# Kernel tuning notes

Hardware: AMD Instinct MI355X
Metric: run time of the kernel (lower is better)

The kernel has to match this reference:

```python
import jax, jax.numpy as jnp
import numpy as np

B, N, M, J, D, PF = 4, 131072, 10475, 55, 64, 486


def setup_inputs() -> dict:
    key = jax.random.key(0)
    ks = jax.random.split(key, 16)
    return {
        "pts": jax.random.normal(ks[0], (B, N, 3), jnp.float32),
        "betas": jax.random.normal(ks[1], (B, 10), jnp.float32),
        "pose_feature": jax.random.normal(ks[2], (B, PF), jnp.float32),
        "init_spdir": jax.random.normal(ks[3], (M, 3, 10), jnp.float32),
        "init_podir": jax.random.normal(ks[4], (PF, 3 * M), jnp.float32),
        "init_faces": jax.random.randint(ks[5], (N, 3), 0, M, jnp.int32),
        "tfs_A": jax.random.normal(ks[6], (B, J, 4, 4), jnp.float32),
        "tfs_inv": jax.random.normal(ks[7], (1, J, 4, 4), jnp.float32),
        "poseoff_cano": jax.random.normal(ks[8], (1, N, 3), jnp.float32),
        "lbsw": jax.random.uniform(ks[9], (1, N, J), jnp.float32),
        "lbs_voxel": jax.random.uniform(ks[10], (1, J, D, D, D), jnp.float32),
        "vox_scale": jnp.ones((1, 1, 3), jnp.float32),
        "vox_offset": jnp.zeros((1, 1, 3), jnp.float32),
        "mask": jax.random.randint(ks[11], (B, N), 0, 2, jnp.int32),
    }


def _trilinear(vox, x, scale, offset):
    # vox: [J,D,D,D], x: [b,n,3] -> [b,n,J] trilinearly interpolated weights
    nj, nd = vox.shape[0], vox.shape[-1]
    g = jnp.clip(x * scale + offset, -1.0, 1.0)          # normalized coords
    t = (g + 1.0) * 0.5 * (nd - 1)                        # voxel coords
    i0 = jnp.clip(jnp.floor(t), 0, nd - 2).astype(jnp.int32)
    f = t - i0                                            # fractional part
    vf = vox.reshape(nj, -1)                              # [J, D^3]
    out = jnp.zeros(x.shape[:-1] + (nj,), x.dtype)
    for dx in (0, 1):
        for dy in (0, 1):
            for dz in (0, 1):
                ix = i0[..., 0] + dx
                iy = i0[..., 1] + dy
                iz = i0[..., 2] + dz
                wgt = ((f[..., 0] if dx else 1.0 - f[..., 0]) *
                       (f[..., 1] if dy else 1.0 - f[..., 1]) *
                       (f[..., 2] if dz else 1.0 - f[..., 2]))
                fid = (ix * nd + iy) * nd + iz            # flat voxel index [b,n]
                out = out + wgt[..., None] * jnp.moveaxis(vf[:, fid], 0, -1)
    return out


def reference(pts, betas, pose_feature, init_spdir, init_podir, init_faces,
              tfs_A, tfs_inv, poseoff_cano, lbsw, lbs_voxel, vox_scale,
              vox_offset, mask):
    b, n, _ = pts.shape
    # blend-shape offsets on template vertices
    shape_full = jnp.einsum('bl,mkl->bmk', betas, init_spdir)      # [b,M,3]
    pose_full = (pose_feature @ init_podir).reshape(b, -1, 3)      # [b,M,3]
    # face-vertex gather then average over the 3 vertices of each face
    shape_off = shape_full[:, init_faces].mean(axis=2)             # [b,F,3]
    pose_off = pose_full[:, init_faces].mean(axis=2)               # [b,F,3]
    x = pts + shape_off + pose_off - poseoff_cano                  # canonical pts + offsets
    # voxel-grid skinning-weight lookup at canonical points
    w_vox = _trilinear(lbs_voxel[0], pts, vox_scale, vox_offset)   # [b,n,J]
    w = jnp.where(mask[..., None] > 0, lbsw, w_vox)
    w = w / jnp.clip(w.sum(-1, keepdims=True), 1e-8)
    # per-point blended transforms: A @ A_inv_template
    tfs = tfs_A @ tfs_inv                                          # [b,J,4,4]
    T = jnp.einsum('bnj,bjrc->bnrc', w, tfs)                       # [b,n,4,4]
    xh = jnp.concatenate([x, jnp.ones_like(x[..., :1])], axis=-1)
    posed = jnp.einsum('bnrc,bnc->bnr', T, xh)[..., :3]
    return posed.reshape(b, n, 1, 3), T
```

## Files before the change

kernel.cpp:

```cpp
#include <hip/hip_runtime.h>

#define B_  4
#define N_  131072
#define J_  55
#define JP_ 56
#define D_  64
#define D3_ 262144
#define PF_ 486
#define COLS_ 31425

#define GZ_ 2048
#define OZ_ 123
#define PZ_ 14336

#define BL16(u) __uint_as_float((u) << 16)
#define BH16(u) __uint_as_float((u) & 0xffff0000u)

typedef float f4a __attribute__((ext_vector_type(4), aligned(4)));

__device__ __forceinline__ unsigned short f2bf(float v) {
    unsigned u = __float_as_uint(v);
    u += 0x7fffu + ((u >> 16) & 1u);
    return (unsigned short)(u >> 16);
}

__device__ __forceinline__ void stage_tfs_bf16(int b, int tid,
                                               const float* __restrict__ A,
                                               const float* __restrict__ Ainv,
                                               unsigned* __restrict__ dst) {
#pragma unroll
    for (int base = 0; base < 448; base += 256) {
        int idx = base + tid;
        if (idx < 448) {
            int j = idx >> 3, pp = idx & 7;
            float e0 = 0.f, e1 = 0.f;
            if (j < J_) {
                int r = pp >> 1, c0 = (pp & 1) * 2;
#pragma unroll
                for (int k = 0; k < 4; ++k) {
                    float av = A[((b * J_ + j) * 4 + r) * 4 + k];
                    e0 += av * Ainv[(j * 4 + k) * 4 + c0];
                    e1 += av * Ainv[(j * 4 + k) * 4 + c0 + 1];
                }
            }
            dst[idx] = (unsigned)f2bf(e0) | ((unsigned)f2bf(e1) << 16);
        }
    }
}

#define UNP16(t, q0, q1)                                        \
    t[0]  = BL16(q0.x); t[1]  = BH16(q0.x);                     \
    t[2]  = BL16(q0.y); t[3]  = BH16(q0.y);                     \
    t[4]  = BL16(q0.z); t[5]  = BH16(q0.z);                     \
    t[6]  = BL16(q0.w); t[7]  = BH16(q0.w);                     \
    t[8]  = BL16(q1.x); t[9]  = BH16(q1.x);                     \
    t[10] = BL16(q1.y); t[11] = BH16(q1.y);                     \
    t[12] = BL16(q1.z); t[13] = BH16(q1.z);                     \
    t[14] = BL16(q1.w); t[15] = BH16(q1.w);

__global__ __launch_bounds__(256) void k_prelude(
    const float* __restrict__ A, const float* __restrict__ Ainv,
    const float* __restrict__ vox,
    uint4* __restrict__ Gtb, float* __restrict__ Stb,
    const float* __restrict__ pf, const float* __restrict__ podir,
    const float* __restrict__ betas, const float* __restrict__ spdir,
    float* __restrict__ off_full,
    const float* __restrict__ lbsw, unsigned* __restrict__ lbswP32) {
    int bx = blockIdx.x;
    int tid = threadIdx.x;

    if (bx < GZ_) {
        __shared__ unsigned stfsb[448];
        int b = (bx & 7) >> 1;
        int chunk = ((bx >> 3) << 1) | (bx & 1);
        stage_tfs_bf16(b, tid, A, Ainv, stfsb);
        __syncthreads();

        int v0 = chunk * 512 + tid;
        float g0[16], g1[16];
#pragma unroll
        for (int r = 0; r < 16; ++r) { g0[r] = 0.f; g1[r] = 0.f; }
        float s0 = 0.f, s1 = 0.f;
        const uint4* s16 = (const uint4*)stfsb;
        float wa[5][2], wb[5][2];
#pragma unroll
        for (int k = 0; k < 5; ++k) {
            wa[k][0] = vox[(size_t)k * D3_ + v0];
            wa[k][1] = vox[(size_t)k * D3_ + v0 + 256];
        }
        for (int j0 = 0; j0 < J_; j0 += 5) {
            if (j0 + 5 < J_) {
#pragma unroll
                for (int k = 0; k < 5; ++k) {
                    wb[k][0] = vox[(size_t)(j0 + 5 + k) * D3_ + v0];
                    wb[k][1] = vox[(size_t)(j0 + 5 + k) * D3_ + v0 + 256];
                }
            }
#pragma unroll
            for (int k = 0; k < 5; ++k) {
                int j = j0 + k;
                uint4 q0 = s16[j * 2], q1 = s16[j * 2 + 1];
                float t[16];
                UNP16(t, q0, q1)
                float w0 = wa[k][0], w1 = wa[k][1];
                s0 += w0; s1 += w1;
#pragma unroll
                for (int r = 0; r < 16; ++r) {
                    g0[r] += w0 * t[r];
                    g1[r] += w1 * t[r];
                }
            }
#pragma unroll
            for (int k = 0; k < 5; ++k) {
                wa[k][0] = wb[k][0]; wa[k][1] = wb[k][1];
            }
        }
        if (b == 0) { Stb[v0] = s0; Stb[v0 + 256] = s1; }
#pragma unroll
        for (int m = 0; m < 2; ++m) {
            float* g = m ? g1 : g0;
            int v = v0 + m * 256;
            unsigned gw[8];
#pragma unroll
            for (int k = 0; k < 8; ++k)
                gw[k] = (unsigned)f2bf(g[2 * k]) |
                        ((unsigned)f2bf(g[2 * k + 1]) << 16);
            uint4* gp = Gtb + ((size_t)b * D3_ + v) * 2;
            gp[0] = make_uint4(gw[0], gw[1], gw[2], gw[3]);
            gp[1] = make_uint4(gw[4], gw[5], gw[6], gw[7]);
        }
    } else if (bx < GZ_ + OZ_) {
        int col = (bx - GZ_) * 256 + tid;
        if (col >= COLS_) return;
        float a0 = 0.f, a1 = 0.f, a2 = 0.f, a3 = 0.f;
        {
            float sp[10];
#pragma unroll
            for (int l = 0; l < 10; ++l) sp[l] = spdir[col * 10 + l];
#pragma unroll
            for (int l = 0; l < 10; ++l) {
                a0 += betas[0 * 10 + l] * sp[l];
                a1 += betas[1 * 10 + l] * sp[l];
                a2 += betas[2 * 10 + l] * sp[l];
                a3 += betas[3 * 10 + l] * sp[l];
            }
        }
        int p = 0;
        for (; p + 16 <= PF_; p += 16) {
            float v16[16];
#pragma unroll
            for (int k = 0; k < 16; ++k)
                v16[k] = podir[(size_t)(p + k) * COLS_ + col];
#pragma unroll
            for (int k = 0; k < 16; ++k) {
                a0 += pf[0 * PF_ + p + k] * v16[k];
                a1 += pf[1 * PF_ + p + k] * v16[k];
                a2 += pf[2 * PF_ + p + k] * v16[k];
                a3 += pf[3 * PF_ + p + k] * v16[k];
            }
        }
        for (; p < PF_; ++p) {
            float v = podir[(size_t)p * COLS_ + col];
            a0 += pf[0 * PF_ + p] * v;
            a1 += pf[1 * PF_ + p] * v;
            a2 += pf[2 * PF_ + p] * v;
            a3 += pf[3 * PF_ + p] * v;
        }
        off_full[0 * COLS_ + col] = a0;
        off_full[1 * COLS_ + col] = a1;
        off_full[2 * COLS_ + col] = a2;
        off_full[3 * COLS_ + col] = a3;
    } else {
        int e = (bx - GZ_ - OZ_) * 256 + tid;
        int n = e / 28;
        int jj = e - n * 28;
        int j0 = 2 * jj;
        float w0 = lbsw[(size_t)n * J_ + j0];
        float w1 = (j0 + 1 < J_) ? lbsw[(size_t)n * J_ + j0 + 1] : 0.f;
        lbswP32[e] = (unsigned)f2bf(w0) | ((unsigned)f2bf(w1) << 16);
    }
}

#define ACC8(Toff, qa, qb)                                 \
    T[Toff + 0] += w0 * BL16(qa.x) + w1 * BL16(qb.x);      \
    T[Toff + 1] += w0 * BH16(qa.x) + w1 * BH16(qb.x);      \
    T[Toff + 2] += w0 * BL16(qa.y) + w1 * BL16(qb.y);      \
    T[Toff + 3] += w0 * BH16(qa.y) + w1 * BH16(qb.y);      \
    T[Toff + 4] += w0 * BL16(qa.z) + w1 * BL16(qb.z);      \
    T[Toff + 5] += w0 * BH16(qa.z) + w1 * BH16(qb.z);      \
    T[Toff + 6] += w0 * BL16(qa.w) + w1 * BL16(qb.w);      \
    T[Toff + 7] += w0 * BH16(qa.w) + w1 * BH16(qb.w);

#define PAIRLOAD(q, sA, sB, f)                             \
    { const uint4* R = Gb + (size_t)(f) * 2;               \
      q[0] = R[0]; q[1] = R[1]; q[2] = R[2]; q[3] = R[3];  \
      sA = Stb[f]; sB = Stb[(f) + 1]; }

#define PAIRCONS(q, sA, sB, wxy)                           \
    { float w0 = (wxy) * wz0, w1 = (wxy) * wz1;            \
      wsum += w0 * sA + w1 * sB;                           \
      uint4 q0 = q[0], q1 = q[1], q2 = q[2], q3 = q[3];    \
      ACC8(0, q0, q2) ACC8(8, q1, q3) }

#define LJACC(jj, wv)                                      \
    { uint4 a0 = s16[(jj) * 2], a1 = s16[(jj) * 2 + 1];    \
      float w = (wv); wsum += w;                           \
      T[0]  += w * BL16(a0.x); T[1]  += w * BH16(a0.x);    \
      T[2]  += w * BL16(a0.y); T[3]  += w * BH16(a0.y);    \
      T[4]  += w * BL16(a0.z); T[5]  += w * BH16(a0.z);    \
      T[6]  += w * BL16(a0.w); T[7]  += w * BH16(a0.w);    \
      T[8]  += w * BL16(a1.x); T[9]  += w * BH16(a1.x);    \
      T[10] += w * BL16(a1.y); T[11] += w * BH16(a1.y);    \
      T[12] += w * BL16(a1.z); T[13] += w * BH16(a1.z);    \
      T[14] += w * BL16(a1.w); T[15] += w * BH16(a1.w); }

__global__ __launch_bounds__(256) void k_main(
    const float* __restrict__ pts, const int* __restrict__ faces,
    const float* __restrict__ poseoff, const int* __restrict__ mask,
    const float* __restrict__ vox_scale, const float* __restrict__ vox_offset,
    const float* __restrict__ off_full,
    const float* __restrict__ A, const float* __restrict__ Ainv,
    const unsigned short* __restrict__ lbswP, const uint4* __restrict__ Gtb,
    const float* __restrict__ Stb,
    float* __restrict__ out_posed, float* __restrict__ out_T) {
    __shared__ float sx0[256], sx1[256], sx2[256];
    __shared__ float sf0[256], sf1[256], sf2[256];
    __shared__ int   scell[256];
    __shared__ unsigned short lst[256];
    __shared__ int wc[4];
    __shared__ unsigned stfsb[448];

    int bid = blockIdx.x;
    int b  = (bid & 7) >> 1;
    int nc = ((bid >> 3) << 1) | (bid & 1);
    int tid = threadIdx.x;
    int n = nc * 256 + tid;
    int i = (b << 17) | n;

    stage_tfs_bf16(b, tid, A, Ainv, stfsb);

    float px = pts[3 * i + 0], py = pts[3 * i + 1], pz = pts[3 * i + 2];
    int f0 = faces[3 * n + 0], f1 = faces[3 * n + 1], f2 = faces[3 * n + 2];
    const float* ob = off_full + b * COLS_;
    const float c3 = 1.f / 3.f;
    f4a o0 = *(const f4a*)(ob + f0 * 3);
    f4a o1 = *(const f4a*)(ob + f1 * 3);
    f4a o2 = *(const f4a*)(ob + f2 * 3);
    float ox = (o0[0] + o1[0] + o2[0]) * c3;
    float oy = (o0[1] + o1[1] + o2[1]) * c3;
    float oz = (o0[2] + o1[2] + o2[2]) * c3;
    sx0[tid] = px + ox - poseoff[3 * n + 0];
    sx1[tid] = py + oy - poseoff[3 * n + 1];
    sx2[tid] = pz + oz - poseoff[3 * n + 2];

    bool isv = !(mask[i] > 0);
    if (isv) {
        float sxc = vox_scale[0], syc = vox_scale[1], szc = vox_scale[2];
        float q0 = vox_offset[0], q1 = vox_offset[1], q2 = vox_offset[2];
        float gx = fminf(fmaxf(px * sxc + q0, -1.f), 1.f);
        float gy = fminf(fmaxf(py * syc + q1, -1.f), 1.f);
        float gz = fminf(fmaxf(pz * szc + q2, -1.f), 1.f);
        float tx = (gx + 1.f) * 0.5f * (D_ - 1);
        float ty = (gy + 1.f) * 0.5f * (D_ - 1);
        float tz = (gz + 1.f) * 0.5f * (D_ - 1);
        int ix = (int)floorf(tx); if (ix > D_ - 2) ix = D_ - 2; if (ix < 0) ix = 0;
        int iy = (int)floorf(ty); if (iy > D_ - 2) iy = D_ - 2; if (iy < 0) iy = 0;
        int iz = (int)floorf(tz); if (iz > D_ - 2) iz = D_ - 2; if (iz < 0) iz = 0;
        sf0[tid] = tx - ix;
        sf1[tid] = ty - iy;
        sf2[tid] = tz - iz;
        scell[tid] = (ix * D_ + iy) * D_ + iz;
    }

    unsigned long long bal = __ballot(isv);
    int lane = tid & 63, wid = tid >> 6;
    if (lane == 0) wc[wid] = __popcll(bal);
    __syncthreads();
    int pre = 0;
#pragma unroll
    for (int k = 0; k < 4; ++k) pre += (k < wid) ? wc[k] : 0;
    int tot = wc[0] + wc[1] + wc[2] + wc[3];
    unsigned long long lt = ((unsigned long long)1 << lane) - 1ull;
    int vbefore = pre + __popcll(bal & lt);
    int pos = isv ? vbefore : (tot + (tid - vbefore));
    lst[pos] = (unsigned short)tid;
    __syncthreads();

    int slot = lst[tid];
    float x0 = sx0[slot], x1 = sx1[slot], x2 = sx2[slot];
    int ii = (b << 17) | (nc * 256 + slot);

    float T[16];
#pragma unroll
    for (int r = 0; r < 16; ++r) T[r] = 0.f;
    float wsum = 0.f;

    if (tid < tot) {
        float fx = sf0[slot], fy = sf1[slot], fz = sf2[slot];
        int cell = scell[slot];
        const uint4* Gb = Gtb + (size_t)b * D3_ * 2;
        float wz0 = 1.f - fz, wz1 = fz;
        float wxy0 = (1.f - fx) * (1.f - fy);
        float wxy1 = (1.f - fx) * fy;
        float wxy2 = fx * (1.f - fy);
        float wxy3 = fx * fy;
        int fid0 = cell;
        int fid1 = cell + D_;
        int fid2 = cell + D_ * D_;
        int fid3 = cell + D_ * D_ + D_;
        uint4 qa[4], qb[4];
        float sa0, sa1, sb0, sb1;
        PAIRLOAD(qa, sa0, sa1, fid0)
        PAIRLOAD(qb, sb0, sb1, fid1)
        PAIRCONS(qa, sa0, sa1, wxy0)
        PAIRLOAD(qa, sa0, sa1, fid2)
        PAIRCONS(qb, sb0, sb1, wxy1)
        PAIRLOAD(qb, sb0, sb1, fid3)
        PAIRCONS(qa, sa0, sa1, wxy2)
        PAIRCONS(qb, sb0, sb1, wxy3)
    } else {
        int n2 = nc * 256 + slot;
        const uint4* lwp = (const uint4*)(lbswP + (size_t)n2 * 56);
        uint4 q[7];
#pragma unroll
        for (int k = 0; k < 7; ++k) q[k] = lwp[k];
        const uint4* s16 = (const uint4*)stfsb;
#pragma unroll
        for (int k = 0; k < 7; ++k) {
            float w8[8];
            w8[0] = BL16(q[k].x); w8[1] = BH16(q[k].x);
            w8[2] = BL16(q[k].y); w8[3] = BH16(q[k].y);
            w8[4] = BL16(q[k].z); w8[5] = BH16(q[k].z);
            w8[6] = BL16(q[k].w); w8[7] = BH16(q[k].w);
#pragma unroll
            for (int m = 0; m < 8; ++m) {
                LJACC(k * 8 + m, w8[m])
            }
        }
    }

    float inv = 1.f / fmaxf(wsum, 1e-8f);
    float t[16];
#pragma unroll
    for (int r = 0; r < 16; ++r) t[r] = T[r] * inv;
    out_posed[3 * ii + 0] = t[0] * x0 + t[1] * x1 + t[2] * x2 + t[3];
    out_posed[3 * ii + 1] = t[4] * x0 + t[5] * x1 + t[6] * x2 + t[7];
    out_posed[3 * ii + 2] = t[8] * x0 + t[9] * x1 + t[10] * x2 + t[11];
    float4* to = (float4*)(out_T + (size_t)ii * 16);
    to[0] = make_float4(t[0], t[1], t[2], t[3]);
    to[1] = make_float4(t[4], t[5], t[6], t[7]);
    to[2] = make_float4(t[8], t[9], t[10], t[11]);
    to[3] = make_float4(t[12], t[13], t[14], t[15]);
}

extern "C" void kernel_launch(void* const* d_in, const int* in_sizes, int n_in,
                              void* d_out, int out_size, void* d_ws, size_t ws_size,
                              hipStream_t stream) {
    const float* pts      = (const float*)d_in[0];
    const float* betas    = (const float*)d_in[1];
    const float* pf       = (const float*)d_in[2];
    const float* spdir    = (const float*)d_in[3];
    const float* podir    = (const float*)d_in[4];
    const int*   faces    = (const int*)d_in[5];
    const float* tfs_A    = (const float*)d_in[6];
    const float* tfs_inv  = (const float*)d_in[7];
    const float* poseoff  = (const float*)d_in[8];
    const float* lbsw     = (const float*)d_in[9];
    const float* vox      = (const float*)d_in[10];
    const float* vscale   = (const float*)d_in[11];
    const float* voffset  = (const float*)d_in[12];
    const int*   mask     = (const int*)d_in[13];

    char* w = (char*)d_ws;
    uint4* Gtb            = (uint4*)w;
    float* Stb            = (float*)(w + 33554432);
    unsigned short* lbswP = (unsigned short*)(w + 34603008);
    float* off_full       = (float*)(w + 49283072);

    float* out_posed = (float*)d_out;
    float* out_T     = out_posed + (size_t)B_ * N_ * 3;

    k_prelude<<<GZ_ + OZ_ + PZ_, 256, 0, stream>>>(
        tfs_A, tfs_inv, vox, Gtb, Stb, pf, podir, betas, spdir, off_full,
        lbsw, (unsigned*)lbswP);
    k_main<<<2048, 256, 0, stream>>>(pts, faces, poseoff, mask, vscale,
                                     voffset, off_full, tfs_A, tfs_inv,
                                     lbswP, Gtb, Stb, out_posed, out_T);
}
```

Measured before the change: 277.2 us.

## Compute voxel-transform grid with bf16 MFMA instead of scalar FMA loops

The prelude stage that precomputes per-voxel blended transforms (55 weights times 16 matrix entries, for each batch) is rewritten as a matrix multiply on the bf16 MFMA 16x16x32 instruction. Each wave loads voxel weights as bf16 A fragments, the transformed tfs are staged transposed in shared memory as B fragments, and results are bounced through shared memory to write packed bf16 output. The grid doubles to 4096 blocks of 64 voxels each. Voxel weights are now rounded to bf16 before accumulation, which adds precision loss. The reuse of sD across batch iterations without a barrier looks racy within a wave, but is probably safe because each wave owns its own slice.

```diff
diff --git a/kernel.cpp b/kernel.cpp
--- a/kernel.cpp
+++ b/kernel.cpp
@@ -9,7 +9,7 @@
 #define PF_ 486
 #define COLS_ 31425
 
-#define GZ_ 2048
+#define GZ_ 4096
 #define OZ_ 123
 #define PZ_ 14336
 
@@ -17,6 +17,8 @@
 #define BH16(u) __uint_as_float((u) & 0xffff0000u)
 
 typedef float f4a __attribute__((ext_vector_type(4), aligned(4)));
+typedef short bf16x8 __attribute__((ext_vector_type(8)));
+typedef float f32x4 __attribute__((ext_vector_type(4)));
 
 __device__ __forceinline__ unsigned short f2bf(float v) {
     unsigned u = __float_as_uint(v);
@@ -47,16 +49,6 @@
         }
     }
 }
-
-#define UNP16(t, q0, q1)                                        \
-    t[0]  = BL16(q0.x); t[1]  = BH16(q0.x);                     \
-    t[2]  = BL16(q0.y); t[3]  = BH16(q0.y);                     \
-    t[4]  = BL16(q0.z); t[5]  = BH16(q0.z);                     \
-    t[6]  = BL16(q0.w); t[7]  = BH16(q0.w);                     \
-    t[8]  = BL16(q1.x); t[9]  = BH16(q1.x);                     \
-    t[10] = BL16(q1.y); t[11] = BH16(q1.y);                     \
-    t[12] = BL16(q1.z); t[13] = BH16(q1.z);                     \
-    t[14] = BL16(q1.w); t[15] = BH16(q1.w);
 
 __global__ __launch_bounds__(256) void k_prelude(
     const float* __restrict__ A, const float* __restrict__ Ainv,
@@ -70,64 +62,70 @@
     int tid = threadIdx.x;
 
     if (bx < GZ_) {
-        __shared__ unsigned stfsb[448];
-        int b = (bx & 7) >> 1;
-        int chunk = ((bx >> 3) << 1) | (bx & 1);
-        stage_tfs_bf16(b, tid, A, Ainv, stfsb);
+        __shared__ short stfsT[4608];
+        __shared__ float sD[4][16][17];
+#pragma unroll
+        for (int it = 0; it < 18; ++it) {
+            int idx = it * 256 + tid;
+            int b = idx / 1152;
+            int rem = idx - b * 1152;
+            int col = rem / 72;
+            int j = rem - col * 72;
+            float e = 0.f;
+            if (j < J_) {
+                int r = col >> 2, c = col & 3;
+#pragma unroll
+                for (int k = 0; k < 4; ++k)
+                    e += A[((b * J_ + j) * 4 + r) * 4 + k] *
+                         Ainv[(j * 4 + k) * 4 + c];
+            }
+            stfsT[idx] = (short)f2bf(e);
+        }
         __syncthreads();
 
-        int v0 = chunk * 512 + tid;
-        float g0[16], g1[16];
-#pragma unroll
-        for (int r = 0; r < 16; ++r) { g0[r] = 0.f; g1[r] = 0.f; }
-        float s0 = 0.f, s1 = 0.f;
-        const uint4* s16 = (const uint4*)stfsb;
-        float wa[5][2], wb[5][2];
-#pragma unroll
-        for (int k = 0; k < 5; ++k) {
-            wa[k][0] = vox[(size_t)k * D3_ + v0];
-            wa[k][1] = vox[(size_t)k * D3_ + v0 + 256];
-        }
-        for (int j0 = 0; j0 < J_; j0 += 5) {
-            if (j0 + 5 < J_) {
-#pragma unroll
-                for (int k = 0; k < 5; ++k) {
-                    wb[k][0] = vox[(size_t)(j0 + 5 + k) * D3_ + v0];
-                    wb[k][1] = vox[(size_t)(j0 + 5 + k) * D3_ + v0 + 256];
-                }
-            }
-#pragma unroll
-            for (int k = 0; k < 5; ++k) {
-                int j = j0 + k;
-                uint4 q0 = s16[j * 2], q1 = s16[j * 2 + 1];
-                float t[16];
-                UNP16(t, q0, q1)
-                float w0 = wa[k][0], w1 = wa[k][1];
-                s0 += w0; s1 += w1;
-#pragma unroll
-                for (int r = 0; r < 16; ++r) {
-                    g0[r] += w0 * t[r];
-                    g1[r] += w1 * t[r];
-                }
-            }
-#pragma unroll
-            for (int k = 0; k < 5; ++k) {
-                wa[k][0] = wb[k][0]; wa[k][1] = wb[k][1];
-            }
-        }
-        if (b == 0) { Stb[v0] = s0; Stb[v0 + 256] = s1; }
-#pragma unroll
-        for (int m = 0; m < 2; ++m) {
-            float* g = m ? g1 : g0;
-            int v = v0 + m * 256;
-            unsigned gw[8];
-#pragma unroll
-            for (int k = 0; k < 8; ++k)
-                gw[k] = (unsigned)f2bf(g[2 * k]) |
-                        ((unsigned)f2bf(g[2 * k + 1]) << 16);
-            uint4* gp = Gtb + ((size_t)b * D3_ + v) * 2;
-            gp[0] = make_uint4(gw[0], gw[1], gw[2], gw[3]);
-            gp[1] = make_uint4(gw[4], gw[5], gw[6], gw[7]);
+        int l = tid & 63, wd = tid >> 6;
+        int vg = bx * 64 + wd * 16 + (l & 15);
+        int jb = (l >> 4) * 8;
+        bf16x8 a0, a1;
+        float sp = 0.f;
+#pragma unroll
+        for (int e = 0; e < 8; ++e) {
+            float f = vox[(size_t)(jb + e) * D3_ + vg];
+            sp += f;
+            a0[e] = (short)f2bf(f);
+        }
+#pragma unroll
+        for (int e = 0; e < 8; ++e) {
+            int j = 32 + jb + e;
+            float f = (j < J_) ? vox[(size_t)j * D3_ + vg] : 0.f;
+            sp += f;
+            a1[e] = (short)f2bf(f);
+        }
+        sp += __shfl_xor(sp, 16);
+        sp += __shfl_xor(sp, 32);
+        if ((l >> 4) == 0) Stb[vg] = sp;
+
+#pragma unroll
+        for (int b = 0; b < 4; ++b) {
+            int col = l & 15;
+            bf16x8 b0 = *(bf16x8*)&stfsT[(b * 16 + col) * 72 + jb];
+            bf16x8 b1 = *(bf16x8*)&stfsT[(b * 16 + col) * 72 + 32 + jb];
+            f32x4 acc = {0.f, 0.f, 0.f, 0.f};
+            acc = __builtin_amdgcn_mfma_f32_16x16x32_bf16(a0, b0, acc, 0, 0, 0);
+            acc = __builtin_amdgcn_mfma_f32_16x16x32_bf16(a1, b1, acc, 0, 0, 0);
+            int row0 = (l >> 4) * 4;
+#pragma unroll
+            for (int r = 0; r < 4; ++r) sD[wd][row0 + r][col] = acc[r];
+            int vloc = l >> 2;
+            int cp = (l & 3) * 4;
+            unsigned w0 = (unsigned)f2bf(sD[wd][vloc][cp + 0]) |
+                          ((unsigned)f2bf(sD[wd][vloc][cp + 1]) << 16);
+            unsigned w1 = (unsigned)f2bf(sD[wd][vloc][cp + 2]) |
+                          ((unsigned)f2bf(sD[wd][vloc][cp + 3]) << 16);
+            int vout = bx * 64 + wd * 16 + vloc;
+            uint2* gp = (uint2*)((unsigned*)Gtb +
+                                 ((size_t)b * D3_ + vout) * 8 + (l & 3) * 2);
+            *gp = make_uint2(w0, w1);
         }
     } else if (bx < GZ_ + OZ_) {
         int col = (bx - GZ_) * 256 + tid;
```

After: 360.8 us. +30.2%, slower.
